# Performance work log

Measured on AMD Instinct MI355X. Metric: run time of the kernel, lower is better.

## Reference

```python
import jax, jax.numpy as jnp
import numpy as np

MAX_SPAN_WIDTH = 12
THRESHOLD = 0.5


def _span_table(num_words):
    starts, ends = [], []
    for s in range(num_words):
        for e in range(s, min(num_words, s + MAX_SPAN_WIDTH)):
            starts.append(s)
            ends.append(e)
    return np.asarray(starts, np.int32), np.asarray(ends, np.int32)


def _mlp(x, w1, b1, w2, b2):
    # Linear -> LeakyReLU(0.01) -> Linear
    return jax.nn.leaky_relu(x @ w1 + b1, negative_slope=0.01) @ w2 + b2


def setup_inputs() -> dict:
    B, L, H, E, W, DFF = 8, 1024, 768, 16, 504, 512
    key = jax.random.key(0)
    ks = jax.random.split(key, 9)
    hidden_states = jax.random.normal(ks[0], (B, L, H), dtype=jnp.float32)
    # layout: first E tokens are entity-type tokens, next 2*W tokens are text (2 subwords/word)
    ent_mask = np.zeros((B, L), np.int32); ent_mask[:, :E] = 1
    text_mask = np.zeros((B, L), np.int32); text_mask[:, E:E + 2 * W] = 1
    word_index = np.full((B, L), -1, np.int32)
    word_index[:, E:E + 2 * W] = np.repeat(np.arange(W, dtype=np.int32), 2)[None, :]
    s = 0.02
    return {
        "hidden_states": hidden_states,
        "ent_w1": jax.random.normal(ks[1], (H, DFF), jnp.float32) * s,
        "ent_b1": jnp.zeros((DFF,), jnp.float32),
        "ent_w2": jax.random.normal(ks[2], (DFF, H), jnp.float32) * s,
        "ent_b2": jnp.zeros((H,), jnp.float32),
        "span_w1": jax.random.normal(ks[3], (2 * H, DFF), jnp.float32) * s,
        "span_b1": jnp.zeros((DFF,), jnp.float32),
        "span_w2": jax.random.normal(ks[4], (DFF, H), jnp.float32) * s,
        "span_b2": jnp.zeros((H,), jnp.float32),
        "text_mask": jnp.asarray(text_mask),
        "ent_mask": jnp.asarray(ent_mask),
        "word_index": jnp.asarray(word_index),
        "num_words": W,
        "num_ent": E,
    }


def reference(hidden_states, ent_w1, ent_b1, ent_w2, ent_b2,
              span_w1, span_b1, span_w2, span_b2,
              text_mask, ent_mask, word_index, num_words, num_ent):
    B, L, H = hidden_states.shape
    W, E = int(num_words), int(num_ent)

    # ---- word-level mean pooling over subword tokens (WordTokenRepresentation) ----
    valid = (text_mask == 1) & (word_index >= 0)                       # [B,L]
    oh = ((word_index[..., None] == jnp.arange(W)) & valid[..., None]).astype(hidden_states.dtype)  # [B,L,W]
    counts = jnp.maximum(oh.sum(axis=1), 1.0)                          # [B,W]
    word_emb = jnp.einsum('blw,blh->bwh', oh, hidden_states) / counts[..., None]

    # ---- gather entity-type tokens in order (EntityTokenRepresentation) ----
    keyv = jnp.where(ent_mask == 1, jnp.arange(L), L + jnp.arange(L))
    ent_pos = jnp.argsort(keyv, axis=-1)[:, :E]                        # [B,E]
    ent_tok = jnp.take_along_axis(hidden_states, ent_pos[..., None], axis=1)  # [B,E,H]
    ent_vec = _mlp(ent_tok, ent_w1, ent_b1, ent_w2, ent_b2)            # [B,E,H]

    # ---- span representations (all spans of width < MAX_SPAN_WIDTH) ----
    starts_np, ends_np = _span_table(W)                                # [N]
    span_in = jnp.concatenate([word_emb[:, starts_np], word_emb[:, ends_np]], axis=-1)  # [B,N,2H]
    span_vec = _mlp(span_in, span_w1, span_b1, span_w2, span_b2)       # [B,N,H]

    # ---- matching logits ----
    logits = jnp.einsum('bnh,beh->bne', span_vec, ent_vec)             # [B,N,E]

    # ---- NMS-style greedy decode (flat mode): threshold + score sort + overlap rejection ----
    N = logits.shape[1]
    probs = jax.nn.sigmoid(logits).reshape(B, N * E)
    cstart = jnp.repeat(jnp.asarray(starts_np), E)                     # [N*E]
    cend = jnp.repeat(jnp.asarray(ends_np), E)
    order = jnp.argsort(-probs, axis=-1)                               # score-descending
    probs_s = jnp.take_along_axis(probs, order, axis=-1)
    s_s, e_s = cstart[order], cend[order]
    pos = jnp.arange(W)

    def decode_one(pr, ss, ee):
        def body(cov, x):
            p, s, e = x
            m = (pos >= s) & (pos <= e)                                # candidate span mask over words
            take = (p > THRESHOLD) & ~jnp.any(cov & m)                 # flat: reject any overlap
            return cov | (m & take), take
        _, taken = jax.lax.scan(body, jnp.zeros((W,), bool), (pr, ss, ee))
        return taken

    taken_sorted = jax.vmap(decode_one)(probs_s, s_s, e_s)             # [B,N*E]
    inv = jnp.argsort(order, axis=-1)
    selected = jnp.take_along_axis(taken_sorted, inv, axis=-1).reshape(B, N, E)
    return logits, selected
```

## Files before the change

kernel.cpp:

```cpp
#include <hip/hip_runtime.h>
#include <hip/hip_bf16.h>
#include <stdint.h>

#define B_ 8
#define L_ 1024
#define H_ 768
#define E_ 16
#define W_ 504
#define DFF_ 512
#define N_ 5982
#define NE_ (N_*E_)
#define BNE_ (B_*NE_)
#define MAXK48 0x0000FFFFFFFFFFFFull
#define PT_ 24

typedef unsigned long long u64;
typedef unsigned int u32;

__device__ __forceinline__ int rowstart_of(int s){
    int s0 = W_ - 11;
    if (s <= s0) return 12*s;
    int t = s - s0;
    return 12*s0 + t*11 - (t*(t-1))/2;
}

__global__ void k_prolog(const int* __restrict__ ent_mask, int* __restrict__ ent_pos,
                         int* __restrict__ starts, int* __restrict__ ends,
                         int* __restrict__ tokc){
    int blk = blockIdx.x; int tid = threadIdx.x;
    if (blk == 8){
        for (int s = tid; s < W_; s += 256){
            int rs = rowstart_of(s);
            int cnt = min(12, W_ - s);
            for (int i = 0; i < cnt; i++){ starts[rs+i] = s; ends[rs+i] = s+i; }
        }
        for (int i = tid; i < B_*W_; i += 256) tokc[i] = 0;
        return;
    }
    __shared__ u32 wt[4]; __shared__ u32 cbase;
    int b = blk;
    int lane = tid & 63, wave = tid >> 6;
    if (tid == 0) cbase = 0;
    __syncthreads();
    for (int base = 0; base < L_; base += 256){
        int l = base + tid;
        bool f = (ent_mask[b*L_ + l] == 1);
        u64 bal = __ballot(f);
        if (lane == 0) wt[wave] = (u32)__popcll(bal);
        __syncthreads();
        u32 pre = cbase;
        for (int w = 0; w < 4; w++) if (w < wave) pre += wt[w];
        if (f){
            u32 rank = pre + (u32)__popcll(bal & ((1ull<<lane)-1ull));
            if (rank < E_) ent_pos[b*E_ + rank] = l;
        }
        __syncthreads();
        if (tid == 0){ u32 r = cbase; for (int w = 0; w < 4; w++) r += wt[w]; cbase = r; }
        __syncthreads();
    }
    u32 totEnt = cbase;
    if (totEnt >= E_) return;
    for (int base = 0; base < L_; base += 256){
        int l = base + tid;
        bool f = (ent_mask[b*L_ + l] != 1);
        u64 bal = __ballot(f);
        if (lane == 0) wt[wave] = (u32)__popcll(bal);
        __syncthreads();
        u32 pre = cbase;
        for (int w = 0; w < 4; w++) if (w < wave) pre += wt[w];
        if (f){
            u32 rank = pre + (u32)__popcll(bal & ((1ull<<lane)-1ull));
            if (rank < E_) ent_pos[b*E_ + rank] = l;
        }
        __syncthreads();
        if (tid == 0){ u32 r = cbase; for (int w = 0; w < 4; w++) r += wt[w]; cbase = r; }
        __syncthreads();
    }
}

__global__ void k_toklist(const int* __restrict__ tm, const int* __restrict__ wi,
                          int* __restrict__ tok, int* __restrict__ tokc){
    int i = blockIdx.x*256 + threadIdx.x;
    if (i >= B_*L_) return;
    int w = wi[i];
    if (tm[i] == 1 && w >= 0 && w < W_){
        int b = i / L_;
        int bw = b*W_ + w;
        int pos = atomicAdd(&tokc[bw], 1);
        if (pos < 4) tok[bw*4 + pos] = i - b*L_;
    }
}

__global__ void k_poolsort(const float* __restrict__ hs, const int* __restrict__ tok,
                           const int* __restrict__ tokc, float* __restrict__ wemb){
    __shared__ int stok[4]; __shared__ int scnt;
    int bw = blockIdx.x;
    int b = bw / W_;
    int tid = threadIdx.x;
    if (tid == 0){
        int c = tokc[bw]; int cc = min(c, 4);
        int v[4];
        for (int k = 0; k < cc; k++) v[k] = tok[bw*4 + k];
        for (int a = 1; a < cc; a++){ int x = v[a]; int j = a-1; while (j >= 0 && v[j] > x){ v[j+1] = v[j]; j--; } v[j+1] = x; }
        for (int k = 0; k < cc; k++) stok[k] = v[k];
        scnt = c;
    }
    __syncthreads();
    int c = scnt; int cc = min(c, 4);
    float denom = (float)max(c, 1);
    for (int h = tid; h < H_; h += 256){
        double s = 0.0;
        for (int k = 0; k < cc; k++)
            s += (double)hs[((size_t)(b*L_ + stok[k]))*H_ + h];
        wemb[(size_t)bw*H_ + h] = (float)(s / (double)denom);
    }
}

__global__ void k_ent(const float* __restrict__ hs, const int* __restrict__ ent_pos,
                      const float* __restrict__ w1, const float* __restrict__ b1,
                      const float* __restrict__ w2, const float* __restrict__ b2,
                      float* __restrict__ ent_vec){
    __shared__ float x[H_];
    __shared__ float hid[DFF_];
    int be = blockIdx.x;
    int b = be >> 4;
    int tid = threadIdx.x;
    int pos = ent_pos[be];
    const float* xp = hs + ((size_t)b*L_ + pos)*H_;
    for (int j = tid; j < H_; j += 256) x[j] = xp[j];
    __syncthreads();
    #pragma unroll
    for (int q = 0; q < 2; q++){
        int d = q*256 + tid;
        float a0=0.f,a1=0.f,a2=0.f,a3=0.f;
        const float* wp = w1 + d;
        #pragma unroll 4
        for (int h = 0; h < H_; h += 4){
            a0 += x[h+0]*wp[(size_t)(h+0)*DFF_];
            a1 += x[h+1]*wp[(size_t)(h+1)*DFF_];
            a2 += x[h+2]*wp[(size_t)(h+2)*DFF_];
            a3 += x[h+3]*wp[(size_t)(h+3)*DFF_];
        }
        float acc = ((a0+a1)+(a2+a3)) + b1[d];
        hid[d] = acc > 0.f ? acc : 0.01f*acc;
    }
    __syncthreads();
    #pragma unroll
    for (int q = 0; q < 3; q++){
        int j = q*256 + tid;
        float a0=0.f,a1=0.f,a2=0.f,a3=0.f;
        const float* wp = w2 + j;
        #pragma unroll 4
        for (int d = 0; d < DFF_; d += 4){
            a0 += hid[d+0]*wp[(size_t)(d+0)*H_];
            a1 += hid[d+1]*wp[(size_t)(d+1)*H_];
            a2 += hid[d+2]*wp[(size_t)(d+2)*H_];
            a3 += hid[d+3]*wp[(size_t)(d+3)*H_];
        }
        ent_vec[(size_t)be*H_ + j] = ((a0+a1)+(a2+a3)) + b2[j];
    }
}

__global__ void k_Mc(const float* __restrict__ span_w2, const float* __restrict__ span_b2,
                     const float* __restrict__ ent_vec, float* __restrict__ M,
                     float* __restrict__ cvec){
    int blk = blockIdx.x;
    if (blk == 256){
        int i = threadIdx.x;
        if (i < B_*E_){
            const float* ev = ent_vec + (size_t)i*H_;
            double acc = 0.0;
            for (int h = 0; h < H_; h++) acc += (double)span_b2[h]*(double)ev[h];
            cvec[i] = (float)acc;
        }
        return;
    }
    int b = blk/32; int dbase = (blk%32)*16;
    int tid = threadIdx.x; int d = dbase + (tid>>4); int e = tid&15;
    const float* ev = ent_vec + ((size_t)b*E_ + e)*H_;
    const float* wr = span_w2 + (size_t)d*H_;
    double p0=0.0, p1=0.0;
    for (int h = 0; h < H_; h += 2){
        p0 += (double)wr[h]*(double)ev[h];
        p1 += (double)wr[h+1]*(double)ev[h+1];
    }
    M[((size_t)b*DFF_ + d)*E_ + e] = (float)(p0+p1);
}

__global__ void k_pq(const float* __restrict__ wemb, const float* __restrict__ w1,
                     float* __restrict__ PQ, int b0){
    __shared__ float As[16][68];
    __shared__ float Bs[16][68];
    int bx = blockIdx.x & 15;
    int by = blockIdx.x >> 4;
    int tid = threadIdx.x;
    int tm = tid >> 4, tn = tid & 15;
    const float* A0 = wemb + (size_t)b0*W_*H_;
    int colbase = bx*64;
    const float* Bbase = (colbase < DFF_) ? w1 : (w1 + (size_t)H_*DFF_);
    int bcol0 = (colbase < DFF_) ? colbase : (colbase - DFF_);
    float acc[4][4] = {{0.f}};
    int ar = tid >> 2, akq = tid & 3;
    int bkk = tid >> 4, bcq = tid & 15;
    const int ROWS = 4*W_;
    for (int k0 = 0; k0 < H_; k0 += 16){
        {
            int gr = by*64 + ar;
            float4 av;
            if (gr < ROWS) av = *(const float4*)(A0 + (size_t)gr*H_ + k0 + akq*4);
            else av = make_float4(0.f,0.f,0.f,0.f);
            As[akq*4+0][ar] = av.x; As[akq*4+1][ar] = av.y;
            As[akq*4+2][ar] = av.z; As[akq*4+3][ar] = av.w;
        }
        {
            float4 bv = *(const float4*)(Bbase + (size_t)(k0+bkk)*DFF_ + bcol0 + bcq*4);
            Bs[bkk][bcq*4+0] = bv.x; Bs[bkk][bcq*4+1] = bv.y;
            Bs[bkk][bcq*4+2] = bv.z; Bs[bkk][bcq*4+3] = bv.w;
        }
        __syncthreads();
        #pragma unroll
        for (int kk = 0; kk < 16; kk++){
            float4 a = *(const float4*)&As[kk][tm*4];
            float4 bv = *(const float4*)&Bs[kk][tn*4];
            acc[0][0] += a.x*bv.x; acc[0][1] += a.x*bv.y; acc[0][2] += a.x*bv.z; acc[0][3] += a.x*bv.w;
            acc[1][0] += a.y*bv.x; acc[1][1] += a.y*bv.y; acc[1][2] += a.y*bv.z; acc[1][3] += a.y*bv.w;
            acc[2][0] += a.z*bv.x; acc[2][1] += a.z*bv.y; acc[2][2] += a.z*bv.z; acc[2][3] += a.z*bv.w;
            acc[3][0] += a.w*bv.x; acc[3][1] += a.w*bv.y; acc[3][2] += a.w*bv.z; acc[3][3] += a.w*bv.w;
        }
        __syncthreads();
    }
    #pragma unroll
    for (int r = 0; r < 4; r++){
        int gr = by*64 + tm*4 + r;
        if (gr < ROWS){
            float4 ov = make_float4(acc[r][0], acc[r][1], acc[r][2], acc[r][3]);
            *(float4*)(PQ + (size_t)gr*1024 + colbase + tn*4) = ov;
        }
    }
}

__global__ void k_logits(const float* __restrict__ PQ, const float* __restrict__ Mmat,
                         const float* __restrict__ cvec, const float* __restrict__ span_b1,
                         float* __restrict__ logits, float* __restrict__ outL, int b0){
    __shared__ float Ps[DFF_];
    __shared__ float hid[DFF_];
    __shared__ double redw[64];
    __shared__ float csh[E_];
    int blk = blockIdx.x;
    int bl = blk / W_; int s = blk - bl*W_;
    int b = b0 + bl;
    int tid = threadIdx.x;
    int lane = tid & 63, wave = tid >> 6;
    int ee = tid & 15; int g = tid >> 4;
    float Mreg[32];
    {
        const float* Mp = Mmat + (size_t)b*DFF_*E_ + (size_t)(g*32)*E_ + ee;
        #pragma unroll
        for (int i = 0; i < 32; i++) Mreg[i] = Mp[(size_t)i*E_];
    }
    const float* P = PQ + ((size_t)(bl*W_ + s))*1024;
    for (int d = tid; d < DFF_; d += 256) Ps[d] = P[d] + span_b1[d];
    if (tid < E_) csh[tid] = cvec[b*E_ + tid];
    __syncthreads();
    int nsp = min(12, W_ - s);
    int nbase = rowstart_of(s);
    for (int i = 0; i < nsp; i++){
        int e = s + i;
        const float* Q = PQ + ((size_t)(bl*W_ + e))*1024 + DFF_;
        for (int d = tid; d < DFF_; d += 256){
            float h = Ps[d] + Q[d];
            hid[d] = h > 0.f ? h : 0.01f*h;
        }
        __syncthreads();
        {
            double acc = 0.0;
            int d0 = g*32;
            #pragma unroll
            for (int k = 0; k < 32; k++) acc += (double)hid[d0+k]*(double)Mreg[k];
            double t = acc + __shfl_down(acc, 32, 64);
            t = t + __shfl_down(t, 16, 64);
            if (lane < 16) redw[wave*16 + lane] = t;
        }
        __syncthreads();
        if (tid < E_){
            double t = ((redw[tid] + redw[16+tid]) + (redw[32+tid] + redw[48+tid]))
                     + (double)csh[tid];
            float lg = (float)t;
            size_t oi = ((size_t)b*N_ + nbase + i)*E_ + tid;
            logits[oi] = lg;
            outL[oi] = lg;
        }
        __syncthreads();
    }
}

__global__ void k_spanbest(const float* __restrict__ logits,
                           const int* __restrict__ starts, const int* __restrict__ ends,
                           u64* __restrict__ candS, float* __restrict__ outSel){
    int idx = blockIdx.x*256 + threadIdx.x;
    if (idx >= B_*N_) return;
    int b = idx / N_; int n = idx - b*N_;
    const float* lg = logits + (size_t)b*NE_ + (size_t)n*16;
    u64 best = ~0ull;
    for (int e = 0; e < 16; e++){
        float prob = 1.0f/(1.0f + expf(-lg[e]));
        if (prob > 0.5f){
            u32 key24 = (~__float_as_uint(prob)) & 0xFFFFFFu;
            u64 pk = ((u64)key24 << 24) | (u64)(u32)(n*16 + e);
            best = best < pk ? best : pk;
        }
    }
    int s = starts[n], e2 = ends[n];
    int len = e2 - s + 1;
    u64 packed = best;
    if (best != ~0ull)
        packed = best | ((u64)(u32)s << 48) | ((u64)(u32)(len-1) << 57);
    candS[idx] = packed;
    float* selp = outSel + (size_t)BNE_ + (size_t)b*NE_ + (size_t)n*16;
    float4 z = make_float4(0.f,0.f,0.f,0.f);
    *(float4*)(selp+0)  = z; *(float4*)(selp+4)  = z;
    *(float4*)(selp+8)  = z; *(float4*)(selp+12) = z;
}

__device__ __forceinline__ void decode_wave(const u64* sp, int n,
                                            float* __restrict__ outSel, int b){
    int lane = threadIdx.x & 63;
    u64 scov[8];
    #pragma unroll
    for (int k = 0; k < 8; k++) scov[k] = 0ull;
    int covcnt = 0;
    for (int base = 0; base < n; base += 64){
        int i = base + lane;
        bool has = i < n;
        u64 v = has ? sp[i] : ~0ull;
        int s   = (int)((v >> 48) & 0x1FFull);
        int len = (int)((v >> 57) & 0xFull) + 1;
        u32 c   = (u32)(v & 0xFFFFFFull);
        int w0 = s >> 6, sh0 = s & 63;
        int w1i = (w0 < 7) ? w0 + 1 : 7;
        u64 full = (1ull << len) - 1ull;
        u64 m0 = has ? (full << sh0) : 0ull;
        u64 m1 = (has && sh0 + len > 64) ? (full >> (64 - sh0)) : 0ull;
        u64 myc0 = 0ull, myc1 = 0ull;
        #pragma unroll
        for (int k = 0; k < 8; k++){
            if (w0  == k) myc0 = scov[k];
            if (w1i == k) myc1 = scov[k];
        }
        bool tent = has && (((myc0 & m0) | (myc1 & m1)) == 0ull);
        u64 bal = __ballot(tent);
        u32 vlo = (u32)v, vhi = (u32)(v >> 32);
        u64 acc = 0ull;
        while (bal){
            int j = (int)__builtin_ctzll(bal);
            bal &= bal - 1ull;
#if __has_builtin(__builtin_amdgcn_readlane)
            u32 jlo = (u32)__builtin_amdgcn_readlane((int)vlo, j);
            u32 jhi = (u32)__builtin_amdgcn_readlane((int)vhi, j);
#else
            u32 jlo = (u32)__shfl((int)vlo, j, 64);
            u32 jhi = (u32)__shfl((int)vhi, j, 64);
#endif
            u64 jv = ((u64)jhi << 32) | (u64)jlo;
            int js   = (int)((jv >> 48) & 0x1FFull);
            int jlen = (int)((jv >> 57) & 0xFull) + 1;
            int jw0 = js >> 6, jsh = js & 63;
            int jw1 = (jw0 < 7) ? jw0 + 1 : 7;
            u64 jfull = (1ull << jlen) - 1ull;
            u64 jm0 = jfull << jsh;
            u64 jm1 = (jsh + jlen > 64) ? (jfull >> (64 - jsh)) : 0ull;
            u64 c0 = 0ull, c1 = 0ull;
            #pragma unroll
            for (int k = 0; k < 8; k++){
                if (jw0 == k) c0 = scov[k];
                if (jw1 == k) c1 = scov[k];
            }
            bool ok = (((c0 & jm0) | (c1 & jm1)) == 0ull);
            u64 okm = ok ? ~0ull : 0ull;
            #pragma unroll
            for (int k = 0; k < 8; k++){
                u64 add = 0ull;
                if (jw0 == k) add |= jm0;
                if (jw1 == k) add |= jm1;
                scov[k] |= (add & okm);
            }
            covcnt += ok ? jlen : 0;
            acc |= (okm & (1ull << j));
        }
        if (((acc >> lane) & 1ull) != 0ull)
            outSel[(size_t)BNE_ + (size_t)b*NE_ + (size_t)c] = 1.0f;
        if (covcnt >= W_) break;
    }
}

__global__ __launch_bounds__(256) void k_tail(const u64* __restrict__ candS,
                                              float* __restrict__ outSel){
    __shared__ u64 cs[6032];
    __shared__ u64 Ma[512], Mb[512];
    __shared__ u32 wtot[4];
    __shared__ int nsh;
    int b = blockIdx.x; int tid = threadIdx.x;
    int lane = tid & 63, wave = tid >> 6;
    const u64* cSg = candS + (size_t)b*N_;

    for (int i = tid; i < N_; i += 256) cs[i] = cSg[i];
    __syncthreads();

    for (int s = tid; s < 512; s += 256)
        Ma[s] = (s < W_) ? (cs[rowstart_of(s)] & MAXK48) : MAXK48;
    __syncthreads();
    u64* Mcur = Ma; u64* Mnext = Mb;
    for (int l = 2; l <= 12; l++){
        #pragma unroll
        for (int q = 0; q < 2; q++){
            int s = tid + q*256;
            u64 key = MAXK48; int idx = -1;
            if (s + l <= W_){ idx = rowstart_of(s) + (l-1); key = cs[idx] & MAXK48; }
            u64 a = Mcur[s];
            u64 bb = (s + 1 < 512) ? Mcur[s+1] : MAXK48;
            u64 dom = a < bb ? a : bb;
            if (idx >= 0 && dom < key) cs[idx] = ~0ull;
            Mnext[s] = dom < key ? dom : key;
        }
        __syncthreads();
        u64* t = Mcur; Mcur = Mnext; Mnext = t;
    }

    {
        int base = tid*PT_;
        u64 vv[PT_];
        u32 flags = 0; int cnt = 0;
        #pragma unroll
        for (int k = 0; k < PT_; k++){
            int i = base + k;
            u64 v = (i < N_) ? cs[i] : ~0ull;
            vv[k] = v;
            if (v != ~0ull){ flags |= (1u << k); cnt++; }
        }
        u32 inc = (u32)cnt;
        for (int d = 1; d < 64; d <<= 1){ u32 o = (u32)__shfl_up((int)inc, d, 64); if (lane >= d) inc += o; }
        if (lane == 63) wtot[wave] = inc;
        __syncthreads();
        u32 woffs = 0;
        for (int w = 0; w < 4; w++) if (w < wave) woffs += wtot[w];
        u32 off = woffs + inc - (u32)cnt;
        if (tid == 255) nsh = (int)(woffs + inc);
        #pragma unroll
        for (int k = 0; k < PT_; k++){
            if (flags & (1u << k)) cs[off++] = vv[k];
        }
    }
    __syncthreads();
    int n = nsh;
    if (tid < 8) cs[n + tid] = ~0ull;
    __syncthreads();

    if (n <= 1024){
        u64 v0=~0ull, v1=~0ull, v2=~0ull, v3=~0ull;
        u64 k0=0, k1=0, k2=0, k3=0;
        if (tid       < n){ v0 = cs[tid];       k0 = v0 & MAXK48; }
        if (tid + 256 < n){ v1 = cs[tid + 256]; k1 = v1 & MAXK48; }
        if (tid + 512 < n){ v2 = cs[tid + 512]; k2 = v2 & MAXK48; }
        if (tid + 768 < n){ v3 = cs[tid + 768]; k3 = v3 & MAXK48; }
        u32 r0=0, r1=0, r2=0, r3=0;
        for (int j = 0; j < n; j += 8){
            u64 c0 = cs[j+0] & MAXK48, c1 = cs[j+1] & MAXK48;
            u64 c2 = cs[j+2] & MAXK48, c3 = cs[j+3] & MAXK48;
            u64 c4 = cs[j+4] & MAXK48, c5 = cs[j+5] & MAXK48;
            u64 c6 = cs[j+6] & MAXK48, c7 = cs[j+7] & MAXK48;
            r0 += (u32)(c0<k0) + (u32)(c1<k0) + (u32)(c2<k0) + (u32)(c3<k0)
                + (u32)(c4<k0) + (u32)(c5<k0) + (u32)(c6<k0) + (u32)(c7<k0);
            r1 += (u32)(c0<k1) + (u32)(c1<k1) + (u32)(c2<k1) + (u32)(c3<k1)
                + (u32)(c4<k1) + (u32)(c5<k1) + (u32)(c6<k1) + (u32)(c7<k1);
            r2 += (u32)(c0<k2) + (u32)(c1<k2) + (u32)(c2<k2) + (u32)(c3<k2)
                + (u32)(c4<k2) + (u32)(c5<k2) + (u32)(c6<k2) + (u32)(c7<k2);
            r3 += (u32)(c0<k3) + (u32)(c1<k3) + (u32)(c2<k3) + (u32)(c3<k3)
                + (u32)(c4<k3) + (u32)(c5<k3) + (u32)(c6<k3) + (u32)(c7<k3);
        }
        __syncthreads();
        if (tid       < n) cs[r0] = v0;
        if (tid + 256 < n) cs[r1] = v1;
        if (tid + 512 < n) cs[r2] = v2;
        if (tid + 768 < n) cs[r3] = v3;
        __syncthreads();
    } else {
        u64 vv[PT_]; u32 rr[PT_];
        #pragma unroll
        for (int k = 0; k < PT_; k++){ vv[k] = ~0ull; rr[k] = 0; }
        #pragma unroll
        for (int k = 0; k < PT_; k++){
            int i = tid + (k << 8);
            if (i < n){
                u64 v = cs[i];
                vv[k] = v;
                u64 ki = v & MAXK48;
                u32 r = 0;
                for (int j = 0; j < n; j += 8){
                    u64 c0 = cs[j+0]&MAXK48, c1 = cs[j+1]&MAXK48;
                    u64 c2 = cs[j+2]&MAXK48, c3 = cs[j+3]&MAXK48;
                    u64 c4 = cs[j+4]&MAXK48, c5 = cs[j+5]&MAXK48;
                    u64 c6 = cs[j+6]&MAXK48, c7 = cs[j+7]&MAXK48;
                    r += (u32)(c0<ki) + (u32)(c1<ki) + (u32)(c2<ki) + (u32)(c3<ki)
                       + (u32)(c4<ki) + (u32)(c5<ki) + (u32)(c6<ki) + (u32)(c7<ki);
                }
                rr[k] = r;
            }
        }
        __syncthreads();
        #pragma unroll
        for (int k = 0; k < PT_; k++){
            int i = tid + (k << 8);
            if (i < n) cs[rr[k]] = vv[k];
        }
        __syncthreads();
    }

    if (wave == 0) decode_wave(cs, n, outSel, b);
}

extern "C" void kernel_launch(void* const* d_in, const int* in_sizes, int n_in,
                              void* d_out, int out_size, void* d_ws, size_t ws_size,
                              hipStream_t stream){
    const float* hs        = (const float*)d_in[0];
    const float* ent_w1    = (const float*)d_in[1];
    const float* ent_b1    = (const float*)d_in[2];
    const float* ent_w2    = (const float*)d_in[3];
    const float* ent_b2    = (const float*)d_in[4];
    const float* span_w1   = (const float*)d_in[5];
    const float* span_b1   = (const float*)d_in[6];
    const float* span_w2   = (const float*)d_in[7];
    const float* span_b2   = (const float*)d_in[8];
    const int*  text_mask  = (const int*)d_in[9];
    const int*  ent_mask   = (const int*)d_in[10];
    const int*  word_index = (const int*)d_in[11];
    float* out = (float*)d_out;

    char* wsbase = (char*)d_ws; size_t off = 0;
    auto alloc = [&](size_t bytes)->void*{ void* p = wsbase + off; off = (off + bytes + 255) & ~(size_t)255; return p; };
    char*  region1 = (char*)alloc((size_t)B_*W_*H_*4);
    float* wemb   = (float*)region1;
    u64*   candS  = (u64*)region1;
    int*   tok    = (int*)  alloc((size_t)B_*W_*4*4);
    int*   tokc   = (int*)  alloc((size_t)B_*W_*4);
    float* PQ     = (float*)alloc((size_t)4*W_*1024*4);
    float* logits = (float*)alloc((size_t)BNE_*4);
    int*   entpos = (int*)  alloc((size_t)B_*E_*4);
    float* entvec = (float*)alloc((size_t)B_*E_*H_*4);
    float* Mmat   = (float*)alloc((size_t)B_*DFF_*E_*4);
    float* cvec   = (float*)alloc((size_t)B_*E_*4);
    int*   starts = (int*)  alloc((size_t)N_*4);
    int*   ends   = (int*)  alloc((size_t)N_*4);

    k_prolog<<<9,256,0,stream>>>(ent_mask, entpos, starts, ends, tokc);
    k_toklist<<<(B_*L_+255)/256,256,0,stream>>>(text_mask, word_index, tok, tokc);
    k_poolsort<<<B_*W_,256,0,stream>>>(hs, tok, tokc, wemb);
    k_ent<<<B_*E_,256,0,stream>>>(hs, entpos, ent_w1, ent_b1, ent_w2, ent_b2, entvec);
    k_Mc<<<257,256,0,stream>>>(span_w2, span_b2, entvec, Mmat, cvec);
    for (int b0 = 0; b0 < B_; b0 += 4){
        k_pq<<<512,256,0,stream>>>(wemb, span_w1, PQ, b0);
        k_logits<<<4*W_,256,0,stream>>>(PQ, Mmat, cvec, span_b1, logits, out, b0);
    }
    k_spanbest<<<(B_*N_+255)/256,256,0,stream>>>(logits, starts, ends, candS, out);
    k_tail<<<B_,256,0,stream>>>(candS, out);
}
```

Baseline: 512.4 us.

## Split entity MLP, prefetch k_pq tiles, and parallelise greedy decode via local minima

```diff
diff --git a/kernel.cpp b/kernel.cpp
--- a/kernel.cpp
+++ b/kernel.cpp
@@ -116,49 +116,53 @@
     }
 }
 
-__global__ void k_ent(const float* __restrict__ hs, const int* __restrict__ ent_pos,
-                      const float* __restrict__ w1, const float* __restrict__ b1,
-                      const float* __restrict__ w2, const float* __restrict__ b2,
-                      float* __restrict__ ent_vec){
+__global__ void k_ent1(const float* __restrict__ hs, const int* __restrict__ ent_pos,
+                       const float* __restrict__ w1, const float* __restrict__ b1,
+                       float* __restrict__ hidg){
     __shared__ float x[H_];
-    __shared__ float hid[DFF_];
-    int be = blockIdx.x;
+    int blk = blockIdx.x;
+    int be = blk >> 1; int half = blk & 1;
     int b = be >> 4;
     int tid = threadIdx.x;
     int pos = ent_pos[be];
     const float* xp = hs + ((size_t)b*L_ + pos)*H_;
     for (int j = tid; j < H_; j += 256) x[j] = xp[j];
     __syncthreads();
-    #pragma unroll
-    for (int q = 0; q < 2; q++){
-        int d = q*256 + tid;
-        float a0=0.f,a1=0.f,a2=0.f,a3=0.f;
-        const float* wp = w1 + d;
-        #pragma unroll 4
-        for (int h = 0; h < H_; h += 4){
-            a0 += x[h+0]*wp[(size_t)(h+0)*DFF_];
-            a1 += x[h+1]*wp[(size_t)(h+1)*DFF_];
-            a2 += x[h+2]*wp[(size_t)(h+2)*DFF_];
-            a3 += x[h+3]*wp[(size_t)(h+3)*DFF_];
-        }
-        float acc = ((a0+a1)+(a2+a3)) + b1[d];
-        hid[d] = acc > 0.f ? acc : 0.01f*acc;
-    }
+    int d = half*256 + tid;
+    float a0=0.f,a1=0.f,a2=0.f,a3=0.f;
+    const float* wp = w1 + d;
+    #pragma unroll 8
+    for (int h = 0; h < H_; h += 4){
+        a0 += x[h+0]*wp[(size_t)(h+0)*DFF_];
+        a1 += x[h+1]*wp[(size_t)(h+1)*DFF_];
+        a2 += x[h+2]*wp[(size_t)(h+2)*DFF_];
+        a3 += x[h+3]*wp[(size_t)(h+3)*DFF_];
+    }
+    float acc = ((a0+a1)+(a2+a3)) + b1[d];
+    hidg[(size_t)be*DFF_ + d] = acc > 0.f ? acc : 0.01f*acc;
+}
+
+__global__ void k_ent2(const float* __restrict__ hidg,
+                       const float* __restrict__ w2, const float* __restrict__ b2,
+                       float* __restrict__ ent_vec){
+    __shared__ float hsd[DFF_];
+    int blk = blockIdx.x;
+    int be = blk / 3; int third = blk % 3;
+    int tid = threadIdx.x;
+    const float* hp = hidg + (size_t)be*DFF_;
+    for (int j = tid; j < DFF_; j += 256) hsd[j] = hp[j];
     __syncthreads();
-    #pragma unroll
-    for (int q = 0; q < 3; q++){
-        int j = q*256 + tid;
-        float a0=0.f,a1=0.f,a2=0.f,a3=0.f;
-        const float* wp = w2 + j;
-        #pragma unroll 4
-        for (int d = 0; d < DFF_; d += 4){
-            a0 += hid[d+0]*wp[(size_t)(d+0)*H_];
-            a1 += hid[d+1]*wp[(size_t)(d+1)*H_];
-            a2 += hid[d+2]*wp[(size_t)(d+2)*H_];
-            a3 += hid[d+3]*wp[(size_t)(d+3)*H_];
-        }
-        ent_vec[(size_t)be*H_ + j] = ((a0+a1)+(a2+a3)) + b2[j];
-    }
+    int j = third*256 + tid;
+    float a0=0.f,a1=0.f,a2=0.f,a3=0.f;
+    const float* wp = w2 + j;
+    #pragma unroll 8
+    for (int d = 0; d < DFF_; d += 4){
+        a0 += hsd[d+0]*wp[(size_t)(d+0)*H_];
+        a1 += hsd[d+1]*wp[(size_t)(d+1)*H_];
+        a2 += hsd[d+2]*wp[(size_t)(d+2)*H_];
+        a3 += hsd[d+3]*wp[(size_t)(d+3)*H_];
+    }
+    ent_vec[(size_t)be*H_ + j] = ((a0+a1)+(a2+a3)) + b2[j];
 }
 
 __global__ void k_Mc(const float* __restrict__ span_w2, const float* __restrict__ span_b2,
@@ -189,8 +193,8 @@
 
 __global__ void k_pq(const float* __restrict__ wemb, const float* __restrict__ w1,
                      float* __restrict__ PQ, int b0){
-    __shared__ float As[16][68];
-    __shared__ float Bs[16][68];
+    __shared__ float As[32][68];
+    __shared__ float Bs[32][68];
     int bx = blockIdx.x & 15;
     int by = blockIdx.x >> 4;
     int tid = threadIdx.x;
@@ -203,23 +207,34 @@
     int ar = tid >> 2, akq = tid & 3;
     int bkk = tid >> 4, bcq = tid & 15;
     const int ROWS = 4*W_;
-    for (int k0 = 0; k0 < H_; k0 += 16){
-        {
-            int gr = by*64 + ar;
-            float4 av;
-            if (gr < ROWS) av = *(const float4*)(A0 + (size_t)gr*H_ + k0 + akq*4);
-            else av = make_float4(0.f,0.f,0.f,0.f);
-            As[akq*4+0][ar] = av.x; As[akq*4+1][ar] = av.y;
-            As[akq*4+2][ar] = av.z; As[akq*4+3][ar] = av.w;
-        }
-        {
-            float4 bv = *(const float4*)(Bbase + (size_t)(k0+bkk)*DFF_ + bcol0 + bcq*4);
-            Bs[bkk][bcq*4+0] = bv.x; Bs[bkk][bcq*4+1] = bv.y;
-            Bs[bkk][bcq*4+2] = bv.z; Bs[bkk][bcq*4+3] = bv.w;
-        }
-        __syncthreads();
+    int gr = by*64 + ar;
+    bool aok = (gr < ROWS);
+    const float* Ap = A0 + (size_t)gr*H_ + akq*4;
+    const float* Bp = Bbase + (size_t)bkk*DFF_ + bcol0 + bcq*4;
+    float4 av0, av1, bv0, bv1;
+    av0 = aok ? *(const float4*)(Ap + 0)  : make_float4(0.f,0.f,0.f,0.f);
+    av1 = aok ? *(const float4*)(Ap + 16) : make_float4(0.f,0.f,0.f,0.f);
+    bv0 = *(const float4*)(Bp + 0);
+    bv1 = *(const float4*)(Bp + (size_t)16*DFF_);
+    for (int k0 = 0; k0 < H_; k0 += 32){
+        As[akq*4+0][ar] = av0.x; As[akq*4+1][ar] = av0.y;
+        As[akq*4+2][ar] = av0.z; As[akq*4+3][ar] = av0.w;
+        As[16+akq*4+0][ar] = av1.x; As[16+akq*4+1][ar] = av1.y;
+        As[16+akq*4+2][ar] = av1.z; As[16+akq*4+3][ar] = av1.w;
+        Bs[bkk][bcq*4+0] = bv0.x; Bs[bkk][bcq*4+1] = bv0.y;
+        Bs[bkk][bcq*4+2] = bv0.z; Bs[bkk][bcq*4+3] = bv0.w;
+        Bs[16+bkk][bcq*4+0] = bv1.x; Bs[16+bkk][bcq*4+1] = bv1.y;
+        Bs[16+bkk][bcq*4+2] = bv1.z; Bs[16+bkk][bcq*4+3] = bv1.w;
+        __syncthreads();
+        if (k0 + 32 < H_){
+            int kn = k0 + 32;
+            av0 = aok ? *(const float4*)(Ap + kn)      : make_float4(0.f,0.f,0.f,0.f);
+            av1 = aok ? *(const float4*)(Ap + kn + 16) : make_float4(0.f,0.f,0.f,0.f);
+            bv0 = *(const float4*)(Bp + (size_t)kn*DFF_);
+            bv1 = *(const float4*)(Bp + (size_t)(kn+16)*DFF_);
+        }
         #pragma unroll
-        for (int kk = 0; kk < 16; kk++){
+        for (int kk = 0; kk < 32; kk++){
             float4 a = *(const float4*)&As[kk][tm*4];
             float4 bv = *(const float4*)&Bs[kk][tn*4];
             acc[0][0] += a.x*bv.x; acc[0][1] += a.x*bv.y; acc[0][2] += a.x*bv.z; acc[0][3] += a.x*bv.w;
@@ -231,10 +246,10 @@
     }
     #pragma unroll
     for (int r = 0; r < 4; r++){
-        int gr = by*64 + tm*4 + r;
-        if (gr < ROWS){
+        int grr = by*64 + tm*4 + r;
+        if (grr < ROWS){
             float4 ov = make_float4(acc[r][0], acc[r][1], acc[r][2], acc[r][3]);
-            *(float4*)(PQ + (size_t)gr*1024 + colbase + tn*4) = ov;
+            *(float4*)(PQ + (size_t)grr*1024 + colbase + tn*4) = ov;
         }
     }
 }
@@ -273,10 +288,16 @@
         }
         __syncthreads();
         {
-            double acc = 0.0;
             int d0 = g*32;
+            double a0=0.0, a1=0.0, a2=0.0, a3=0.0;
             #pragma unroll
-            for (int k = 0; k < 32; k++) acc += (double)hid[d0+k]*(double)Mreg[k];
+            for (int k = 0; k < 32; k += 4){
+                a0 += (double)hid[d0+k+0]*(double)Mreg[k+0];
+                a1 += (double)hid[d0+k+1]*(double)Mreg[k+1];
+                a2 += (double)hid[d0+k+2]*(double)Mreg[k+2];
+                a3 += (double)hid[d0+k+3]*(double)Mreg[k+3];
+            }
+            double acc = (a0+a1)+(a2+a3);
             double t = acc + __shfl_down(acc, 32, 64);
             t = t + __shfl_down(t, 16, 64);
             if (lane < 16) redw[wave*16 + lane] = t;
@@ -322,200 +343,70 @@
     *(float4*)(selp+8)  = z; *(float4*)(selp+12) = z;
 }
 
-__device__ __forceinline__ void decode_wave(const u64* sp, int n,
-                                            float* __restrict__ outSel, int b){
-    int lane = threadIdx.x & 63;
-    u64 scov[8];
-    #pragma unroll
-    for (int k = 0; k < 8; k++) scov[k] = 0ull;
-    int covcnt = 0;
-    for (int base = 0; base < n; base += 64){
-        int i = base + lane;
-        bool has = i < n;
-        u64 v = has ? sp[i] : ~0ull;
-        int s   = (int)((v >> 48) & 0x1FFull);
-        int len = (int)((v >> 57) & 0xFull) + 1;
-        u32 c   = (u32)(v & 0xFFFFFFull);
-        int w0 = s >> 6, sh0 = s & 63;
-        int w1i = (w0 < 7) ? w0 + 1 : 7;
-        u64 full = (1ull << len) - 1ull;
-        u64 m0 = has ? (full << sh0) : 0ull;
-        u64 m1 = (has && sh0 + len > 64) ? (full >> (64 - sh0)) : 0ull;
-        u64 myc0 = 0ull, myc1 = 0ull;
-        #pragma unroll
-        for (int k = 0; k < 8; k++){
-            if (w0  == k) myc0 = scov[k];
-            if (w1i == k) myc1 = scov[k];
-        }
-        bool tent = has && (((myc0 & m0) | (myc1 & m1)) == 0ull);
-        u64 bal = __ballot(tent);
-        u32 vlo = (u32)v, vhi = (u32)(v >> 32);
-        u64 acc = 0ull;
-        while (bal){
-            int j = (int)__builtin_ctzll(bal);
-            bal &= bal - 1ull;
-#if __has_builtin(__builtin_amdgcn_readlane)
-            u32 jlo = (u32)__builtin_amdgcn_readlane((int)vlo, j);
-            u32 jhi = (u32)__builtin_amdgcn_readlane((int)vhi, j);
-#else
-            u32 jlo = (u32)__shfl((int)vlo, j, 64);
-            u32 jhi = (u32)__shfl((int)vhi, j, 64);
-#endif
-            u64 jv = ((u64)jhi << 32) | (u64)jlo;
-            int js   = (int)((jv >> 48) & 0x1FFull);
-            int jlen = (int)((jv >> 57) & 0xFull) + 1;
-            int jw0 = js >> 6, jsh = js & 63;
-            int jw1 = (jw0 < 7) ? jw0 + 1 : 7;
-            u64 jfull = (1ull << jlen) - 1ull;
-            u64 jm0 = jfull << jsh;
-            u64 jm1 = (jsh + jlen > 64) ? (jfull >> (64 - jsh)) : 0ull;
-            u64 c0 = 0ull, c1 = 0ull;
-            #pragma unroll
-            for (int k = 0; k < 8; k++){
-                if (jw0 == k) c0 = scov[k];
-                if (jw1 == k) c1 = scov[k];
-            }
-            bool ok = (((c0 & jm0) | (c1 & jm1)) == 0ull);
-            u64 okm = ok ? ~0ull : 0ull;
-            #pragma unroll
-            for (int k = 0; k < 8; k++){
-                u64 add = 0ull;
-                if (jw0 == k) add |= jm0;
-                if (jw1 == k) add |= jm1;
-                scov[k] |= (add & okm);
-            }
-            covcnt += ok ? jlen : 0;
-            acc |= (okm & (1ull << j));
-        }
-        if (((acc >> lane) & 1ull) != 0ull)
-            outSel[(size_t)BNE_ + (size_t)b*NE_ + (size_t)c] = 1.0f;
-        if (covcnt >= W_) break;
-    }
-}
-
 __global__ __launch_bounds__(256) void k_tail(const u64* __restrict__ candS,
                                               float* __restrict__ outSel){
-    __shared__ u64 cs[6032];
-    __shared__ u64 Ma[512], Mb[512];
-    __shared__ u32 wtot[4];
-    __shared__ int nsh;
+    __shared__ u64 cs[6144];
+    __shared__ u64 mcov[512];
+    __shared__ u32 ckey[512];
     int b = blockIdx.x; int tid = threadIdx.x;
-    int lane = tid & 63, wave = tid >> 6;
     const u64* cSg = candS + (size_t)b*N_;
-
-    for (int i = tid; i < N_; i += 256) cs[i] = cSg[i];
-    __syncthreads();
-
-    for (int s = tid; s < 512; s += 256)
-        Ma[s] = (s < W_) ? (cs[rowstart_of(s)] & MAXK48) : MAXK48;
-    __syncthreads();
-    u64* Mcur = Ma; u64* Mnext = Mb;
-    for (int l = 2; l <= 12; l++){
-        #pragma unroll
-        for (int q = 0; q < 2; q++){
-            int s = tid + q*256;
-            u64 key = MAXK48; int idx = -1;
-            if (s + l <= W_){ idx = rowstart_of(s) + (l-1); key = cs[idx] & MAXK48; }
-            u64 a = Mcur[s];
-            u64 bb = (s + 1 < 512) ? Mcur[s+1] : MAXK48;
-            u64 dom = a < bb ? a : bb;
-            if (idx >= 0 && dom < key) cs[idx] = ~0ull;
-            Mnext[s] = dom < key ? dom : key;
-        }
-        __syncthreads();
-        u64* t = Mcur; Mcur = Mnext; Mnext = t;
-    }
-
-    {
-        int base = tid*PT_;
-        u64 vv[PT_];
-        u32 flags = 0; int cnt = 0;
-        #pragma unroll
-        for (int k = 0; k < PT_; k++){
-            int i = base + k;
-            u64 v = (i < N_) ? cs[i] : ~0ull;
-            vv[k] = v;
-            if (v != ~0ull){ flags |= (1u << k); cnt++; }
-        }
-        u32 inc = (u32)cnt;
-        for (int d = 1; d < 64; d <<= 1){ u32 o = (u32)__shfl_up((int)inc, d, 64); if (lane >= d) inc += o; }
-        if (lane == 63) wtot[wave] = inc;
-        __syncthreads();
-        u32 woffs = 0;
-        for (int w = 0; w < 4; w++) if (w < wave) woffs += wtot[w];
-        u32 off = woffs + inc - (u32)cnt;
-        if (tid == 255) nsh = (int)(woffs + inc);
-        #pragma unroll
-        for (int k = 0; k < PT_; k++){
-            if (flags & (1u << k)) cs[off++] = vv[k];
-        }
-    }
-    __syncthreads();
-    int n = nsh;
-    if (tid < 8) cs[n + tid] = ~0ull;
-    __syncthreads();
-
-    if (n <= 1024){
-        u64 v0=~0ull, v1=~0ull, v2=~0ull, v3=~0ull;
-        u64 k0=0, k1=0, k2=0, k3=0;
-        if (tid       < n){ v0 = cs[tid];       k0 = v0 & MAXK48; }
-        if (tid + 256 < n){ v1 = cs[tid + 256]; k1 = v1 & MAXK48; }
-        if (tid + 512 < n){ v2 = cs[tid + 512]; k2 = v2 & MAXK48; }
-        if (tid + 768 < n){ v3 = cs[tid + 768]; k3 = v3 & MAXK48; }
-        u32 r0=0, r1=0, r2=0, r3=0;
-        for (int j = 0; j < n; j += 8){
-            u64 c0 = cs[j+0] & MAXK48, c1 = cs[j+1] & MAXK48;
-            u64 c2 = cs[j+2] & MAXK48, c3 = cs[j+3] & MAXK48;
-            u64 c4 = cs[j+4] & MAXK48, c5 = cs[j+5] & MAXK48;
-            u64 c6 = cs[j+6] & MAXK48, c7 = cs[j+7] & MAXK48;
-            r0 += (u32)(c0<k0) + (u32)(c1<k0) + (u32)(c2<k0) + (u32)(c3<k0)
-                + (u32)(c4<k0) + (u32)(c5<k0) + (u32)(c6<k0) + (u32)(c7<k0);
-            r1 += (u32)(c0<k1) + (u32)(c1<k1) + (u32)(c2<k1) + (u32)(c3<k1)
-                + (u32)(c4<k1) + (u32)(c5<k1) + (u32)(c6<k1) + (u32)(c7<k1);
-            r2 += (u32)(c0<k2) + (u32)(c1<k2) + (u32)(c2<k2) + (u32)(c3<k2)
-                + (u32)(c4<k2) + (u32)(c5<k2) + (u32)(c6<k2) + (u32)(c7<k2);
-            r3 += (u32)(c0<k3) + (u32)(c1<k3) + (u32)(c2<k3) + (u32)(c3<k3)
-                + (u32)(c4<k3) + (u32)(c5<k3) + (u32)(c6<k3) + (u32)(c7<k3);
-        }
-        __syncthreads();
-        if (tid       < n) cs[r0] = v0;
-        if (tid + 256 < n) cs[r1] = v1;
-        if (tid + 512 < n) cs[r2] = v2;
-        if (tid + 768 < n) cs[r3] = v3;
-        __syncthreads();
-    } else {
-        u64 vv[PT_]; u32 rr[PT_];
-        #pragma unroll
-        for (int k = 0; k < PT_; k++){ vv[k] = ~0ull; rr[k] = 0; }
-        #pragma unroll
-        for (int k = 0; k < PT_; k++){
-            int i = tid + (k << 8);
-            if (i < n){
-                u64 v = cs[i];
-                vv[k] = v;
-                u64 ki = v & MAXK48;
-                u32 r = 0;
-                for (int j = 0; j < n; j += 8){
-                    u64 c0 = cs[j+0]&MAXK48, c1 = cs[j+1]&MAXK48;
-                    u64 c2 = cs[j+2]&MAXK48, c3 = cs[j+3]&MAXK48;
-                    u64 c4 = cs[j+4]&MAXK48, c5 = cs[j+5]&MAXK48;
-                    u64 c6 = cs[j+6]&MAXK48, c7 = cs[j+7]&MAXK48;
-                    r += (u32)(c0<ki) + (u32)(c1<ki) + (u32)(c2<ki) + (u32)(c3<ki)
-                       + (u32)(c4<ki) + (u32)(c5<ki) + (u32)(c6<ki) + (u32)(c7<ki);
-                }
-                rr[k] = r;
+    u32 alive = 0;
+    #pragma unroll
+    for (int k = 0; k < PT_; k++){
+        int i = tid + (k << 8);
+        u64 v = (i < N_) ? cSg[i] : ~0ull;
+        cs[i] = v;
+        if (v != ~0ull) alive |= (1u << k);
+    }
+    while (true){
+        mcov[tid] = ~0ull; mcov[tid+256] = ~0ull;
+        ckey[tid] = 0u;    ckey[tid+256] = 0u;
+        __syncthreads();
+        u32 am = alive;
+        while (am){
+            int k = __builtin_ctz(am); am &= am - 1u;
+            u64 v = cs[tid + (k << 8)];
+            int s   = (int)((v >> 48) & 0x1FFull);
+            int len = (int)((v >> 57) & 0xFull) + 1;
+            u64 key = v & MAXK48;
+            for (int w = s; w < s + len; w++)
+                atomicMin(&mcov[w], key);
+        }
+        __syncthreads();
+        u32 accm = 0;
+        am = alive;
+        while (am){
+            int k = __builtin_ctz(am); am &= am - 1u;
+            u64 v = cs[tid + (k << 8)];
+            int s   = (int)((v >> 48) & 0x1FFull);
+            int len = (int)((v >> 57) & 0xFull) + 1;
+            u64 key = v & MAXK48;
+            u64 rmin = ~0ull;
+            for (int w = s; w < s + len; w++){ u64 t = mcov[w]; if (t < rmin) rmin = t; }
+            if (rmin == key){
+                accm |= (1u << k);
+                for (int w = s; w < s + len; w++) ckey[w] = 1u;
+                u32 c = (u32)(v & 0xFFFFFFull);
+                outSel[(size_t)BNE_ + (size_t)b*NE_ + (size_t)c] = 1.0f;
             }
         }
-        __syncthreads();
-        #pragma unroll
-        for (int k = 0; k < PT_; k++){
-            int i = tid + (k << 8);
-            if (i < n) cs[rr[k]] = vv[k];
-        }
-        __syncthreads();
-    }
-
-    if (wave == 0) decode_wave(cs, n, outSel, b);
+        alive &= ~accm;
+        __syncthreads();
+        u32 killm = 0;
+        am = alive;
+        while (am){
+            int k = __builtin_ctz(am); am &= am - 1u;
+            u64 v = cs[tid + (k << 8)];
+            int s   = (int)((v >> 48) & 0x1FFull);
+            int len = (int)((v >> 57) & 0xFull) + 1;
+            u32 f = 0;
+            for (int w = s; w < s + len; w++) f |= ckey[w];
+            if (f) killm |= (1u << k);
+        }
+        alive &= ~killm;
+        int na = __syncthreads_count(alive != 0u);
+        if (na == 0) break;
+    }
 }
 
 extern "C" void kernel_launch(void* const* d_in, const int* in_sizes, int n_in,
@@ -545,6 +436,7 @@
     float* PQ     = (float*)alloc((size_t)4*W_*1024*4);
     float* logits = (float*)alloc((size_t)BNE_*4);
     int*   entpos = (int*)  alloc((size_t)B_*E_*4);
+    float* hidg   = (float*)alloc((size_t)B_*E_*DFF_*4);
     float* entvec = (float*)alloc((size_t)B_*E_*H_*4);
     float* Mmat   = (float*)alloc((size_t)B_*DFF_*E_*4);
     float* cvec   = (float*)alloc((size_t)B_*E_*4);
@@ -554,7 +446,8 @@
     k_prolog<<<9,256,0,stream>>>(ent_mask, entpos, starts, ends, tokc);
     k_toklist<<<(B_*L_+255)/256,256,0,stream>>>(text_mask, word_index, tok, tokc);
     k_poolsort<<<B_*W_,256,0,stream>>>(hs, tok, tokc, wemb);
-    k_ent<<<B_*E_,256,0,stream>>>(hs, entpos, ent_w1, ent_b1, ent_w2, ent_b2, entvec);
+    k_ent1<<<B_*E_*2,256,0,stream>>>(hs, entpos, ent_w1, ent_b1, hidg);
+    k_ent2<<<B_*E_*3,256,0,stream>>>(hidg, ent_w2, ent_b2, entvec);
     k_Mc<<<257,256,0,stream>>>(span_w2, span_b2, entvec, Mmat, cvec);
     for (int b0 = 0; b0 < B_; b0 += 4){
         k_pq<<<512,256,0,stream>>>(wemb, span_w1, PQ, b0);
```

Result: faster. 418.3 us (-18.4%).
